# Kernel tuning notes

Hardware: AMD Instinct MI355X
Metric: run time of the kernel (lower is better)

Reference implementation:

```python
import jax, jax.numpy as jnp
import numpy as np

WINDOW_SIZE = 11
SIGMA = 1.5
C1 = 0.01 ** 2
C2 = 0.03 ** 2
LAMBDA_DSSIM = 0.2


def _gaussian_window(channel):
    x = jnp.arange(WINDOW_SIZE, dtype=jnp.float32)
    g = jnp.exp(-((x - WINDOW_SIZE // 2) ** 2) / (2.0 * SIGMA ** 2))
    g = g / g.sum()
    w2d = jnp.outer(g, g)  # [ws, ws]
    # depthwise kernel: [O=C, I=1, ws, ws]
    return jnp.broadcast_to(w2d[None, None], (channel, 1, WINDOW_SIZE, WINDOW_SIZE))


def _dwconv(x, window, channel):
    # x: [1, C, H, W]; same padding ws//2, depthwise (groups=C)
    pad = WINDOW_SIZE // 2
    return jax.lax.conv_general_dilated(
        x, window,
        window_strides=(1, 1),
        padding=((pad, pad), (pad, pad)),
        dimension_numbers=("NCHW", "OIHW", "NCHW"),
        feature_group_count=channel,
    )


def _ssim_mean(img1, img2):
    # img1, img2: [C, H, W]
    channel = img1.shape[0]
    window = _gaussian_window(channel).astype(img1.dtype)
    a = img1[None]  # [1, C, H, W]
    b = img2[None]

    mu1 = _dwconv(a, window, channel)
    mu2 = _dwconv(b, window, channel)
    mu1_sq = mu1 * mu1
    mu2_sq = mu2 * mu2
    mu1_mu2 = mu1 * mu2
    sigma1_sq = _dwconv(a * a, window, channel) - mu1_sq
    sigma2_sq = _dwconv(b * b, window, channel) - mu2_sq
    sigma12 = _dwconv(a * b, window, channel) - mu1_mu2

    ssim_map = ((2 * mu1_mu2 + C1) * (2 * sigma12 + C2)) / (
        (mu1_sq + mu2_sq + C1) * (sigma1_sq + sigma2_sq + C2))
    return ssim_map.mean()


def setup_inputs() -> dict:
    key = jax.random.key(0)
    k1, k2 = jax.random.split(key)
    shape = (3, 2160, 3840)
    pred = jax.random.uniform(k1, shape, dtype=jnp.float32)
    target = jax.random.uniform(k2, shape, dtype=jnp.float32)
    return {"pred": pred, "target": target}


def reference(pred, target):
    l1 = jnp.abs(pred - target).mean()
    ssim_val = _ssim_mean(pred, target)
    return (1.0 - LAMBDA_DSSIM) * l1 + LAMBDA_DSSIM * (1.0 - ssim_val)
```

## Files before the change

kernel.cpp:

```cpp
#include <hip/hip_runtime.h>
#include <math.h>

#define WSZ 11
#define PAD 5
#define TX 64
#define TY 16
#define NY 9
#define IY (TY + 2*PAD)
#define RX 4
#define CHX (TX / RX)
#define NTASK0 (IY * CHX)
#define NTASK1 (TY * CHX)
#define SEG (RX + 2*PAD)
#define RY 4
#define SA 65

typedef float v2f __attribute__((ext_vector_type(2)));

struct W11 { float w[WSZ]; };

__global__ __launch_bounds__(256, 4) void ssim_l1_kernel(
    const float* __restrict__ pred, const float* __restrict__ targ,
    W11 wt, float2* __restrict__ partials)
{
    constexpr int H = 2160, W = 3840;
    __shared__ float4 sHA[IY][SA];

    const int c    = blockIdx.z;
    const int gx0  = blockIdx.x * TX;
    const int base = blockIdx.y * (TY * NY);
    const size_t plane = (size_t)H * W;
    const float* p = pred + (size_t)c * plane;
    const float* t = targ + (size_t)c * plane;

    const int tid = threadIdx.x;
    v2f loss_acc = {0.f, 0.f};
    const float C1v = 0.0001f, C2v = 0.0009f;

    const int oxB  = tid & 63;
    const int oy0B = (tid >> 6) * RY;
    const bool xfast = (blockIdx.x >= 1) && (blockIdx.x <= (W / TX) - 2);

    for (int s = 0; s < NY; ++s) {
        if (s > 0) {
            for (int i = tid; i < 2 * PAD * TX; i += 256) {
                const int dr = i >> 6, cc = i & 63;
                sHA[dr][cc] = sHA[dr + TY][cc];
            }
            __syncthreads();
        }

        const int ntask  = (s == 0) ? NTASK0 : NTASK1;
        const int rowoff = (s == 0) ? 0 : 2 * PAD;
        const int gyA    = base + TY * s - PAD;
        for (int task = tid; task < ntask; task += 256) {
            const int r  = task >> 4;
            const int cx = task & 15;
            const int rr = rowoff + r;
            const int gy = gyA + rr;
            const int gxs = gx0 + cx * RX - PAD;
            const bool rowok   = (gy >= 0) && (gy < H);
            const bool own_row = (gy >= base) && (gy < base + TY * NY);

            float4 P[5], T[5];
            if (rowok && xfast) {
                const float4* p4 = (const float4*)(p + (size_t)gy * W + (gxs - 3));
                const float4* t4 = (const float4*)(t + (size_t)gy * W + (gxs - 3));
                #pragma unroll
                for (int i = 0; i < 5; ++i) { P[i] = p4[i]; T[i] = t4[i]; }
            } else if (rowok) {
                const size_t rowoff2 = (size_t)gy * W;
                #pragma unroll
                for (int i = 0; i < 5; ++i) {
                    float pe[4], te[4];
                    #pragma unroll
                    for (int q = 0; q < 4; ++q) {
                        int gx = gxs - 3 + 4 * i + q;
                        bool ok = (gx >= 0) && (gx < W);
                        pe[q] = ok ? p[rowoff2 + gx] : 0.f;
                        te[q] = ok ? t[rowoff2 + gx] : 0.f;
                    }
                    P[i] = make_float4(pe[0], pe[1], pe[2], pe[3]);
                    T[i] = make_float4(te[0], te[1], te[2], te[3]);
                }
            } else {
                #pragma unroll
                for (int i = 0; i < 5; ++i) {
                    P[i] = make_float4(0.f, 0.f, 0.f, 0.f);
                    T[i] = make_float4(0.f, 0.f, 0.f, 0.f);
                }
            }

            v2f h_sd[RX], h_qq[RX];
            #pragma unroll
            for (int j = 0; j < RX; ++j) {
                h_sd[j] = (v2f){0.f, 0.f};
                h_qq[j] = (v2f){0.f, 0.f};
            }
            #pragma unroll
            for (int e = 0; e < SEG; ++e) {
                const int ii = (e + 3) >> 2, qq = (e + 3) & 3;
                const float pe = (qq == 0) ? P[ii].x : (qq == 1) ? P[ii].y
                                : (qq == 2) ? P[ii].z : P[ii].w;
                const float te = (qq == 0) ? T[ii].x : (qq == 1) ? T[ii].y
                                : (qq == 2) ? T[ii].z : T[ii].w;
                v2f vsd; vsd.x = pe + te; vsd.y = pe - te;
                const v2f vsq = vsd * vsd;
                #pragma unroll
                for (int j = 0; j < RX; ++j) {
                    const int k = e - j;
                    if (k >= 0 && k < WSZ) {
                        const float wv = wt.w[k];
                        h_sd[j] += wv * vsd;
                        h_qq[j] += wv * vsq;
                    }
                }
                if (e >= PAD && e < PAD + RX && own_row)
                    loss_acc.y += fabsf(vsd.y);
            }
            const int xb = cx * RX;
            #pragma unroll
            for (int j = 0; j < RX; ++j)
                sHA[rr][xb + j] = make_float4(h_sd[j].x, h_sd[j].y,
                                              h_qq[j].x, h_qq[j].y);
        }
        __syncthreads();

        {
            v2f mu[RY], qq[RY];
            #pragma unroll
            for (int j = 0; j < RY; ++j) {
                mu[j] = (v2f){0.f, 0.f};
                qq[j] = (v2f){0.f, 0.f};
            }
            #pragma unroll
            for (int k = 0; k < RY + 2 * PAD; ++k) {
                const float4 f = sHA[oy0B + k][oxB];
                v2f fsd; fsd.x = f.x; fsd.y = f.y;
                v2f fsq; fsq.x = f.z; fsq.y = f.w;
                #pragma unroll
                for (int j = 0; j < RY; ++j) {
                    const int kk = k - j;
                    if (kk >= 0 && kk < WSZ) {
                        const float wv = wt.w[kk];
                        mu[j] += wv * fsd;
                        qq[j] += wv * fsq;
                    }
                }
            }
            #pragma unroll
            for (int j = 0; j < RY; ++j) {
                const v2f musq = mu[j] * mu[j];
                const v2f rr2  = qq[j] - musq;
                const float a    = 0.5f * (musq.x - musq.y) + C1v;
                const float b    = 0.5f * (rr2.x - rr2.y) + C2v;
                const float cden = 0.5f * (musq.x + musq.y) + C1v;
                const float dden = 0.5f * (rr2.x + rr2.y) + C2v;
                loss_acc.x += (a * b) * __builtin_amdgcn_rcpf(cden * dden);
            }
        }
        __syncthreads();
    }

    #pragma unroll
    for (int off = 32; off > 0; off >>= 1) {
        loss_acc.x += __shfl_down(loss_acc.x, off, 64);
        loss_acc.y += __shfl_down(loss_acc.y, off, 64);
    }
    __shared__ float red[2][4];
    const int lane = tid & 63;
    const int wid  = tid >> 6;
    if (lane == 0) { red[0][wid] = loss_acc.x; red[1][wid] = loss_acc.y; }
    __syncthreads();
    if (tid == 0) {
        const float sv = red[0][0] + red[0][1] + red[0][2] + red[0][3];
        const float lv = red[1][0] + red[1][1] + red[1][2] + red[1][3];
        const int bid = (blockIdx.z * gridDim.y + blockIdx.y) * gridDim.x + blockIdx.x;
        partials[bid] = make_float2(sv, lv);
    }
}

__global__ __launch_bounds__(256) void finalize_kernel(
    const float2* __restrict__ partials, int n,
    float* __restrict__ out, double invN)
{
    const int tid = threadIdx.x;
    double s = 0.0, l = 0.0;
    for (int i = tid; i < n; i += 256) {
        float2 v = partials[i];
        s += (double)v.x;
        l += (double)v.y;
    }
    #pragma unroll
    for (int off = 32; off > 0; off >>= 1) {
        s += __shfl_down(s, off, 64);
        l += __shfl_down(l, off, 64);
    }
    __shared__ double rs[4], rl[4];
    const int lane = tid & 63, wid = tid >> 6;
    if (lane == 0) { rs[wid] = s; rl[wid] = l; }
    __syncthreads();
    if (tid == 0) {
        const double st = rs[0] + rs[1] + rs[2] + rs[3];
        const double lt = rl[0] + rl[1] + rl[2] + rl[3];
        out[0] = (float)(0.8 * lt * invN + 0.2 * (1.0 - st * invN));
    }
}

extern "C" void kernel_launch(void* const* d_in, const int* in_sizes, int n_in,
                              void* d_out, int out_size, void* d_ws, size_t ws_size,
                              hipStream_t stream)
{
    const float* pred = (const float*)d_in[0];
    const float* targ = (const float*)d_in[1];
    float* out = (float*)d_out;
    float2* partials = (float2*)d_ws;

    const int C = 3, H = 2160, W = 3840;

    W11 wt;
    double g[WSZ], sg = 0.0;
    for (int i = 0; i < WSZ; ++i) {
        double d = (double)i - (WSZ / 2);
        g[i] = exp(-(d * d) / (2.0 * 1.5 * 1.5));
        sg += g[i];
    }
    for (int i = 0; i < WSZ; ++i) wt.w[i] = (float)(g[i] / sg);

    dim3 grid(W / TX, H / (TY * NY), C);
    ssim_l1_kernel<<<grid, 256, 0, stream>>>(pred, targ, wt, partials);

    const int nblocks = (W / TX) * (H / (TY * NY)) * C;
    double invN = 1.0 / ((double)C * (double)H * (double)W);
    finalize_kernel<<<1, 256, 0, stream>>>(partials, nblocks, out, invN);
}
```

Before: 251.9 us.

## Replace shared-memory vertical pass with register ring-buffer streaming over row chunks

The vertical blur moves out of a shared-memory tile with halo copies and into a per-thread register ring buffer. Horizontal results for 8 rows at a time are streamed through shared memory, and each pair of threads splits the mean and square channels and exchanges them with a lane shuffle. Tiles widen to 128 columns and 72 output rows per block, and the copy of the halo rows between steps is removed. Every thread now evaluates the SSIM expression twice, once per pair, so the finalize kernel scales the sum by half. The ring adds register pressure and duplicates the SSIM arithmetic in exchange for fewer shared-memory reads and syncs.

```diff
diff --git a/kernel.cpp b/kernel.cpp
--- a/kernel.cpp
+++ b/kernel.cpp
@@ -3,17 +3,14 @@
 
 #define WSZ 11
 #define PAD 5
-#define TX 64
-#define TY 16
-#define NY 9
-#define IY (TY + 2*PAD)
+#define TX 128
+#define RB 72
+#define CR 8
+#define NTILE 11
 #define RX 4
 #define CHX (TX / RX)
-#define NTASK0 (IY * CHX)
-#define NTASK1 (TY * CHX)
 #define SEG (RX + 2*PAD)
-#define RY 4
-#define SA 65
+#define SA 129
 
 typedef float v2f __attribute__((ext_vector_type(2)));
 
@@ -24,11 +21,11 @@
     W11 wt, float2* __restrict__ partials)
 {
     constexpr int H = 2160, W = 3840;
-    __shared__ float4 sHA[IY][SA];
+    __shared__ float4 sH[CR][SA];
 
     const int c    = blockIdx.z;
     const int gx0  = blockIdx.x * TX;
-    const int base = blockIdx.y * (TY * NY);
+    const int base = blockIdx.y * RB;
     const size_t plane = (size_t)H * W;
     const float* p = pred + (size_t)c * plane;
     const float* t = targ + (size_t)c * plane;
@@ -37,30 +34,23 @@
     v2f loss_acc = {0.f, 0.f};
     const float C1v = 0.0001f, C2v = 0.0009f;
 
-    const int oxB  = tid & 63;
-    const int oy0B = (tid >> 6) * RY;
+    const int rA  = tid >> 5;
+    const int cxA = tid & 31;
+    const int u  = tid >> 1;
+    const int ch = tid & 1;
     const bool xfast = (blockIdx.x >= 1) && (blockIdx.x <= (W / TX) - 2);
 
-    for (int s = 0; s < NY; ++s) {
-        if (s > 0) {
-            for (int i = tid; i < 2 * PAD * TX; i += 256) {
-                const int dr = i >> 6, cc = i & 63;
-                sHA[dr][cc] = sHA[dr + TY][cc];
-            }
-            __syncthreads();
-        }
-
-        const int ntask  = (s == 0) ? NTASK0 : NTASK1;
-        const int rowoff = (s == 0) ? 0 : 2 * PAD;
-        const int gyA    = base + TY * s - PAD;
-        for (int task = tid; task < ntask; task += 256) {
-            const int r  = task >> 4;
-            const int cx = task & 15;
-            const int rr = rowoff + r;
-            const int gy = gyA + rr;
-            const int gxs = gx0 + cx * RX - PAD;
+    v2f ring[16];
+    #pragma unroll
+    for (int i = 0; i < 16; ++i) ring[i] = (v2f){0.f, 0.f};
+
+    for (int s = 0; s < NTILE; ++s) {
+        {
+            const int hr  = CR * s + rA;
+            const int gy  = base - PAD + hr;
+            const int gxs = gx0 + cxA * RX - PAD;
             const bool rowok   = (gy >= 0) && (gy < H);
-            const bool own_row = (gy >= base) && (gy < base + TY * NY);
+            const bool own_row = (gy >= base) && (gy < base + RB);
 
             float4 P[5], T[5];
             if (rowok && xfast) {
@@ -118,45 +108,64 @@
                 if (e >= PAD && e < PAD + RX && own_row)
                     loss_acc.y += fabsf(vsd.y);
             }
-            const int xb = cx * RX;
             #pragma unroll
             for (int j = 0; j < RX; ++j)
-                sHA[rr][xb + j] = make_float4(h_sd[j].x, h_sd[j].y,
-                                              h_qq[j].x, h_qq[j].y);
+                sH[rA][j * 32 + cxA] = make_float4(h_sd[j].x, h_sd[j].y,
+                                                   h_qq[j].x, h_qq[j].y);
         }
         __syncthreads();
 
-        {
-            v2f mu[RY], qq[RY];
-            #pragma unroll
-            for (int j = 0; j < RY; ++j) {
-                mu[j] = (v2f){0.f, 0.f};
-                qq[j] = (v2f){0.f, 0.f};
-            }
-            #pragma unroll
-            for (int k = 0; k < RY + 2 * PAD; ++k) {
-                const float4 f = sHA[oy0B + k][oxB];
-                v2f fsd; fsd.x = f.x; fsd.y = f.y;
-                v2f fsq; fsq.x = f.z; fsq.y = f.w;
-                #pragma unroll
-                for (int j = 0; j < RY; ++j) {
-                    const int kk = k - j;
-                    if (kk >= 0 && kk < WSZ) {
-                        const float wv = wt.w[kk];
-                        mu[j] += wv * fsd;
-                        qq[j] += wv * fsq;
-                    }
-                }
-            }
-            #pragma unroll
-            for (int j = 0; j < RY; ++j) {
-                const v2f musq = mu[j] * mu[j];
-                const v2f rr2  = qq[j] - musq;
-                const float a    = 0.5f * (musq.x - musq.y) + C1v;
-                const float b    = 0.5f * (rr2.x - rr2.y) + C2v;
-                const float cden = 0.5f * (musq.x + musq.y) + C1v;
-                const float dden = 0.5f * (rr2.x + rr2.y) + C2v;
-                loss_acc.x += (a * b) * __builtin_amdgcn_rcpf(cden * dden);
+        if (s & 1) {
+            #pragma unroll
+            for (int r = 0; r < CR; ++r) {
+                const v2f* pv = reinterpret_cast<const v2f*>(&sH[r][u]);
+                const v2f h = pv[ch];
+                ring[(8 + r) & 15] = wt.w[0] * h;
+                #pragma unroll
+                for (int d = 1; d <= 10; ++d)
+                    ring[(8 + r - d + 16) & 15] += wt.w[d] * h;
+                const int o = CR * s + r - 10;
+                if ((unsigned)o < (unsigned)RB) {
+                    const v2f own = ring[(8 + r + 6) & 15];
+                    v2f oth;
+                    oth.x = __shfl_xor(own.x, 1, 64);
+                    oth.y = __shfl_xor(own.y, 1, 64);
+                    const v2f mu = ch ? oth : own;
+                    const v2f qv = ch ? own : oth;
+                    const v2f musq = mu * mu;
+                    const v2f rr2  = qv - musq;
+                    const float a    = 0.5f * (musq.x - musq.y) + C1v;
+                    const float b    = 0.5f * (rr2.x - rr2.y) + C2v;
+                    const float cden = 0.5f * (musq.x + musq.y) + C1v;
+                    const float dden = 0.5f * (rr2.x + rr2.y) + C2v;
+                    loss_acc.x += (a * b) * __builtin_amdgcn_rcpf(cden * dden);
+                }
+            }
+        } else {
+            #pragma unroll
+            for (int r = 0; r < CR; ++r) {
+                const v2f* pv = reinterpret_cast<const v2f*>(&sH[r][u]);
+                const v2f h = pv[ch];
+                ring[r & 15] = wt.w[0] * h;
+                #pragma unroll
+                for (int d = 1; d <= 10; ++d)
+                    ring[(r - d + 16) & 15] += wt.w[d] * h;
+                const int o = CR * s + r - 10;
+                if ((unsigned)o < (unsigned)RB) {
+                    const v2f own = ring[(r + 6) & 15];
+                    v2f oth;
+                    oth.x = __shfl_xor(own.x, 1, 64);
+                    oth.y = __shfl_xor(own.y, 1, 64);
+                    const v2f mu = ch ? oth : own;
+                    const v2f qv = ch ? own : oth;
+                    const v2f musq = mu * mu;
+                    const v2f rr2  = qv - musq;
+                    const float a    = 0.5f * (musq.x - musq.y) + C1v;
+                    const float b    = 0.5f * (rr2.x - rr2.y) + C2v;
+                    const float cden = 0.5f * (musq.x + musq.y) + C1v;
+                    const float dden = 0.5f * (rr2.x + rr2.y) + C2v;
+                    loss_acc.x += (a * b) * __builtin_amdgcn_rcpf(cden * dden);
+                }
             }
         }
         __syncthreads();
@@ -203,7 +212,7 @@
     if (tid == 0) {
         const double st = rs[0] + rs[1] + rs[2] + rs[3];
         const double lt = rl[0] + rl[1] + rl[2] + rl[3];
-        out[0] = (float)(0.8 * lt * invN + 0.2 * (1.0 - st * invN));
+        out[0] = (float)(0.8 * lt * invN + 0.2 * (1.0 - 0.5 * st * invN));
     }
 }
 
@@ -227,10 +236,10 @@
     }
     for (int i = 0; i < WSZ; ++i) wt.w[i] = (float)(g[i] / sg);
 
-    dim3 grid(W / TX, H / (TY * NY), C);
+    dim3 grid(W / TX, H / RB, C);
     ssim_l1_kernel<<<grid, 256, 0, stream>>>(pred, targ, wt, partials);
 
-    const int nblocks = (W / TX) * (H / (TY * NY)) * C;
+    const int nblocks = (W / TX) * (H / RB) * C;
     double invN = 1.0 / ((double)C * (double)H * (double)W);
     finalize_kernel<<<1, 256, 0, stream>>>(partials, nblocks, out, invN);
 }
```

Result: slower. 271.2 us (+7.7%).
